# Optimization experiments

Measured on AMD Instinct MI355X. Metric: run time of the kernel, lower is better.

Reference implementation:

```python
import jax, jax.numpy as jnp
import numpy as np

NUM_HEADS = 16
HEAD_DIM = 64
BATCH = 4
SEQ = 1024
MAX_SEQ_LEN = 2048


def _shift(pos_score):
    # Transformer-XL relative shift. pos_score: (NH, S, S_kv)
    NH, S, S_kv = pos_score.shape
    zero_pad = jnp.zeros((NH, S, 1), dtype=pos_score.dtype)
    padded = jnp.concatenate([zero_pad, pos_score], axis=-1)  # (NH, S, S_kv+1)
    padded = padded.reshape(NH, S_kv + 1, S)
    return padded[:, 1:, :].reshape(NH, S, S_kv)


def setup_inputs() -> dict:
    key = jax.random.key(0)
    ks = jax.random.split(key, 6)
    NH = BATCH * NUM_HEADS
    return {
        "queries": jax.random.normal(ks[0], (NH, SEQ, HEAD_DIM), dtype=jnp.float32),
        "keys": jax.random.normal(ks[1], (NH, SEQ, HEAD_DIM), dtype=jnp.float32),
        "values": jax.random.normal(ks[2], (NH, SEQ, HEAD_DIM), dtype=jnp.float32),
        "u_bias": jax.random.normal(ks[3], (1, NUM_HEADS, 1, HEAD_DIM), dtype=jnp.float32),
        "v_bias": jax.random.normal(ks[4], (1, NUM_HEADS, 1, HEAD_DIM), dtype=jnp.float32),
        "R": jax.random.normal(ks[5], (NUM_HEADS, MAX_SEQ_LEN, HEAD_DIM), dtype=jnp.float32),
    }


def reference(queries, keys, values, u_bias, v_bias, R):
    NH, S, d = queries.shape
    S_kv = keys.shape[1]
    batch = NH // NUM_HEADS

    q = queries * (d ** -0.5)
    q = q.reshape(batch, NUM_HEADS, S, d)
    q_u = (q + u_bias).reshape(NH, S, d)
    q_v = (q + v_bias).reshape(NH, S, d)

    # relative position embeddings, tiled over batch: (NH, S_kv, d)
    R_s = jnp.tile(R[:, :S_kv, :], (batch, 1, 1))

    content_score = jnp.einsum('nsd,ntd->nst', q_u, keys)   # (NH, S, S_kv)
    pos_score = jnp.einsum('nsd,ntd->nst', q_v, R_s)        # (NH, S, S_kv)
    pos_score = _shift(pos_score)

    attn_weights = jax.nn.softmax(content_score + pos_score, axis=-1)
    attn = jnp.einsum('nst,ntd->nsd', attn_weights, values)  # (NH, S, d)
    return attn
```

## Files before the change

### kernel.cpp

```cpp
#include <hip/hip_runtime.h>


#define SQ    1024
#define HD    64
#define NHD   16
#define RMAX  2048

typedef _Float16 f16x8 __attribute__((ext_vector_type(8)));
typedef _Float16 f16x4 __attribute__((ext_vector_type(4)));
typedef short    b16x8 __attribute__((ext_vector_type(8)));
typedef short    b16x4 __attribute__((ext_vector_type(4)));
typedef float    f32x4 __attribute__((ext_vector_type(4)));
typedef unsigned u32x2 __attribute__((ext_vector_type(2)));

#define MFMA_F16(A,B,C)  __builtin_amdgcn_mfma_f32_16x16x32_f16((A),(B),(C),0,0,0)
#define MFMA_BF16(A,B,C) __builtin_amdgcn_mfma_f32_16x16x32_bf16((A),(B),(C),0,0,0)

#define L2E    1.44269504088896f
#define NSHIFT (-57.7078016f)

#define KH_OFF   0
#define VT_OFF   (8u << 20)
#define R16_OFF  (18u << 20)
#define WS_NEED  (20u << 20)

__device__ __forceinline__ float exp2fast(float x) {
#if __has_builtin(__builtin_amdgcn_exp2f)
  return __builtin_amdgcn_exp2f(x);
#else
  return __expf(x * 0.693147180559945f);
#endif
}

__device__ __forceinline__ f32x4 mfma16bf(b16x4 a, b16x4 b, f32x4 c) {
#if __has_builtin(__builtin_amdgcn_mfma_f32_16x16x16bf16_1k)
  return __builtin_amdgcn_mfma_f32_16x16x16bf16_1k(a, b, c, 0, 0, 0);
#else
  b16x8 az = {a[0], a[1], a[2], a[3], 0, 0, 0, 0};
  b16x8 bz = {b[0], b[1], b[2], b[3], 0, 0, 0, 0};
  return MFMA_BF16(az, bz, c);
#endif
}

__device__ __forceinline__ short f2b(float f) {
  unsigned u = __builtin_bit_cast(unsigned, f);
  u += 0x7FFFu + ((u >> 16) & 1u);
  return (short)(u >> 16);
}
__device__ __forceinline__ unsigned pkh(float a, float b) {
  _Float16 h0 = (_Float16)a, h1 = (_Float16)b;
  return (unsigned)__builtin_bit_cast(unsigned short, h0)
       | ((unsigned)__builtin_bit_cast(unsigned short, h1) << 16);
}
__device__ __forceinline__ unsigned pkb2(float a, float b) {
  unsigned ua = __builtin_bit_cast(unsigned, a) + 0x8000u;
  unsigned ub = __builtin_bit_cast(unsigned, b) + 0x8000u;
  return (ub & 0xFFFF0000u) | (ua >> 16);
}
__device__ __forceinline__ float h2f(unsigned w, int sh) {
  return (float)__builtin_bit_cast(_Float16, (unsigned short)(w >> sh));
}
__device__ __forceinline__ int swz(int row, int col) {
  return row*64 + ((((col >> 3) ^ row) & 7) << 3) + (col & 7);
}
__device__ __forceinline__ int swzv(int row, int col) {
  return row*64 + ((((col >> 3) ^ row) & 7) << 3)
       + ((col & 7) ^ ((row & 8) >> 1));
}


__global__ __launch_bounds__(256) void preprep(
    const float* __restrict__ K, const float* __restrict__ R,
    const float* __restrict__ V,
    _Float16* __restrict__ Kh, _Float16* __restrict__ R16,
    short* __restrict__ Vt)
{
  __shared__ float t[64][65];
  const int bid = blockIdx.x, tid = threadIdx.x;
  if (bid < 1024) {
    const int n = bid >> 4, st = bid & 15;
    {
      const int row = tid >> 2, c0 = (tid & 3) * 16;
      const float* src = V + ((size_t)n * SQ + st * 64 + row) * HD + c0;
#pragma unroll
      for (int i = 0; i < 4; ++i) {
        float4 x = ((const float4*)src)[i];
        t[row][c0 + 4*i + 0] = x.x; t[row][c0 + 4*i + 1] = x.y;
        t[row][c0 + 4*i + 2] = x.z; t[row][c0 + 4*i + 3] = x.w;
      }
    }
    __syncthreads();
    {
      const int d = tid >> 2, s0 = (tid & 3) * 16;
      short* dst = Vt + ((size_t)n * 80 + d) * SQ + st * 64 + s0;
#pragma unroll
      for (int i = 0; i < 8; ++i)
        *(unsigned*)(dst + 2*i) = pkb2(t[s0 + 2*i][d], t[s0 + 2*i + 1][d]);
    }
    if (tid < 64) {
      const int s = st * 64 + tid;
      Vt[((size_t)n * 80 + 64) * SQ + s] = (short)0x3F80;
#pragma unroll
      for (int r = 65; r < 80; ++r) Vt[((size_t)n * 80 + r) * SQ + s] = 0;
    }
  } else {
    const int idx = (bid - 1024) * 256 + tid;
    const int nk4 = (64 * SQ * HD) / 4;
    if (idx < nk4) {
      float4 v = ((const float4*)K)[idx];
      f16x4 o = { (_Float16)v.x, (_Float16)v.y, (_Float16)v.z, (_Float16)v.w };
      *(f16x4*)(Kh + 4 * (size_t)idx) = o;
    } else {
      int rr = idx - nk4;
      int h  = rr >> 14, off = rr & 16383;
      float4 v = ((const float4*)R)[((size_t)h << 15) + off];
      f16x4 o = { (_Float16)v.x, (_Float16)v.y, (_Float16)v.z, (_Float16)v.w };
      *(f16x4*)(R16 + 4 * (((size_t)h << 14) + off)) = o;
    }
  }
}


__global__ __launch_bounds__(256, 3) void relpos_sdpa_r16(
    const float* __restrict__ Q, const _Float16* __restrict__ Kh,
    const short* __restrict__ Vtg, const _Float16* __restrict__ R16,
    const float* __restrict__ Ub, const float* __restrict__ Vb,
    float* __restrict__ O)
{
  const int n    = blockIdx.x;
  const int h    = n & (NHD - 1);
  const int a0   = blockIdx.y * 64;
  const int tid  = threadIdx.x;
  const int lane = tid & 63, wave = tid >> 6;
  const int l15  = lane & 15, quad = lane >> 4;

  const float*    Qn  = Q   + (size_t)n * SQ * HD;
  const _Float16* Khn = Kh  + (size_t)n * SQ * HD;
  const short*    Vgn = Vtg + (size_t)n * 80 * SQ;
  const _Float16* Rh  = R16 + (size_t)h * SQ * HD;

  __shared__ __align__(16) char lds[33808];
  _Float16*       Kb   = (_Float16*)lds;
  short*          Vt   = (short*)(lds + 8192);
  unsigned*       Pb2  = (unsigned*)(lds + 16384);
  const _Float16* Pb2h = (const _Float16*)Pb2;

  f16x8 quF[2], qvF[5][2];
#pragma unroll
  for (int ks = 0; ks < 2; ++ks) {
    const int db = ks * 32 + quad * 8;
    float ub[8], vb[8];
#pragma unroll
    for (int j = 0; j < 8; ++j) {
      ub[j] = Ub[h*HD + db + j] * L2E;
      vb[j] = Vb[h*HD + db + j] * L2E;
    }
    {
      const float* p = Qn + (size_t)(a0 + 16*wave + l15) * HD + db;
      float4 x0 = ((const float4*)p)[0], x1 = ((const float4*)p)[1];
      f16x8 f;
#pragma unroll
      for (int t = 0; t < 4; ++t) {
        f[t]   = (_Float16)((&x0.x)[t] * (0.125f * L2E) + ub[t]);
        f[t+4] = (_Float16)((&x1.x)[t] * (0.125f * L2E) + ub[t+4]);
      }
      quF[ks] = f;
    }
#pragma unroll
    for (int rt = 0; rt < 5; ++rt) {
      int row = a0 + 16*rt + l15; if (row > SQ-1) row = SQ-1;
      const float* p = Qn + (size_t)row * HD + db;
      float4 x0 = ((const float4*)p)[0], x1 = ((const float4*)p)[1];
      f16x8 f;
#pragma unroll
      for (int t = 0; t < 4; ++t) {
        f[t]   = (_Float16)((&x0.x)[t] * (0.125f * L2E) + vb[t]);
        f[t+4] = (_Float16)((&x1.x)[t] * (0.125f * L2E) + vb[t+4]);
      }
      qvF[rt][ks] = f;
    }
  }

  f32x4 Oacc[4], acc_l;
#pragma unroll
  for (int ct = 0; ct < 4; ++ct) Oacc[ct] = (f32x4){0.f, 0.f, 0.f, 0.f};
  acc_l = (f32x4){0.f, 0.f, 0.f, 0.f};

  const b16x4 ONESB = {(short)0x3F80, (short)0x3F80, (short)0x3F80, (short)0x3F80};

  unsigned ringW[9];
  int ringSlot, ringSlotN;
  f16x8 bB0, bB1;
  auto bandLoad = [&](int jstart) {
    const int c = jstart + 16*wave + l15;
    const int j = (c + 2048) & (SQ - 1);
    ringSlotN   = (c + 2048) & 127;
    const _Float16* rp = Rh + (size_t)j * HD + quad * 8;
    bB0 = *(const f16x8*)rp;
    bB1 = *(const f16x8*)(rp + 32);
  };
  auto bandMFMA = [&]() {
    ringSlot = ringSlotN;
    __builtin_amdgcn_s_setprio(1);
#pragma unroll
    for (int rt = 0; rt < 5; ++rt) {
      f32x4 acc = (f32x4){0.f, 0.f, 0.f, 0.f};
      acc = MFMA_F16(qvF[rt][0], bB0, acc);
      acc = MFMA_F16(qvF[rt][1], bB1, acc);
      if (rt < 4) {
        ringW[2*rt]     = pkh(acc[0], acc[1]);
        ringW[2*rt + 1] = pkh(acc[2], acc[3]);
      } else {
        ringW[8] = pkh(acc[0], acc[1]);
      }
    }
    __builtin_amdgcn_s_setprio(0);
  };
  auto ringFlush = [&]() {
#pragma unroll
    for (int rt = 0; rt < 4; ++rt) {
      const int rp0 = 8*rt + 2*quad;
      Pb2[rp0*132 + ringSlot]       = ringW[2*rt];
      Pb2[(rp0 + 1)*132 + ringSlot] = ringW[2*rt + 1];
    }
    if (quad == 0) Pb2[32*132 + ringSlot] = ringW[8];
    if (ringSlot < 3) {
      const int ms = ringSlot + 128;
#pragma unroll
      for (int rt = 0; rt < 4; ++rt) {
        const int rp0 = 8*rt + 2*quad;
        Pb2[rp0*132 + ms]       = ringW[2*rt];
        Pb2[(rp0 + 1)*132 + ms] = ringW[2*rt + 1];
      }
      if (quad == 0) Pb2[32*132 + ms] = ringW[8];
    }
  };

  bandLoad(-a0 - 65);  bandMFMA();  ringFlush();
  bandLoad(-a0 - 1);   bandMFMA();  ringFlush();

  f16x8 kPre[2]; b16x8 vPre[2];
  auto stageLoad = [&](int k0) {
    const _Float16* ks = Khn + (size_t)(k0 + lane) * HD + wave*8;
    kPre[0] = *(const f16x8*)ks;
    kPre[1] = *(const f16x8*)(ks + 32);
    const short* vs = Vgn + (size_t)lane * SQ + k0 + wave*8;
    vPre[0] = *(const b16x8*)vs;
    vPre[1] = *(const b16x8*)(vs + 32);
  };
  auto stageWrite = [&]() {
    *(f16x8*)&Kb[swz(lane, wave*8)]      = kPre[0];
    *(f16x8*)&Kb[swz(lane, 32 + wave*8)] = kPre[1];
    const int hx = (lane & 8) >> 1;
    const int c0 = ((wave       ^ lane) & 7) << 3;
    const int c1 = (((wave + 4) ^ lane) & 7) << 3;
    short* vr = &Vt[lane * 64];
    b16x8 v0 = vPre[0], v1 = vPre[1];
    b16x4 v0lo = {v0[0], v0[1], v0[2], v0[3]};
    b16x4 v0hi = {v0[4], v0[5], v0[6], v0[7]};
    b16x4 v1lo = {v1[0], v1[1], v1[2], v1[3]};
    b16x4 v1hi = {v1[4], v1[5], v1[6], v1[7]};
    *(b16x4*)&vr[c0 + hx]       = v0lo;
    *(b16x4*)&vr[c0 + (4 ^ hx)] = v0hi;
    *(b16x4*)&vr[c1 + hx]       = v1lo;
    *(b16x4*)&vr[c1 + (4 ^ hx)] = v1hi;
  };

  stageLoad(0);

  const int iiB = 16*wave + 4*quad;
  const int iQ  = 16*wave + l15;

  for (int k0 = 0; k0 < SQ; k0 += 64) {
    __syncthreads();

    stageWrite();
    if (k0 > 0) ringFlush();

    __syncthreads();

    if (k0 < SQ - 64) {
      stageLoad(k0 + 64);
      bandLoad(k0 + 64 - a0 - 1);
    }

    f32x4 sc[4];
    __builtin_amdgcn_s_setprio(1);
#pragma unroll
    for (int ct = 0; ct < 4; ++ct) {
      f16x8 ka = *(const f16x8*)&Kb[swz(16*ct + l15, quad*8)];
      f16x8 kb = *(const f16x8*)&Kb[swz(16*ct + l15, 32 + quad*8)];
      f32x4 acc = (f32x4){NSHIFT, NSHIFT, NSHIFT, NSHIFT};
      acc = MFMA_F16(ka, quF[0], acc);
      acc = MFMA_F16(kb, quF[1], acc);
      sc[ct] = acc;
    }
    __builtin_amdgcn_s_setprio(0);

    const int base = k0 - a0 - 16*wave;
    if (k0 == a0 || k0 == a0 + 64) {
      const int adA = (iQ >> 1) * 264 + (iQ & 1);
      const int adB = ((iQ + 1) >> 1) * 264 + ((iQ + 1) & 1);
#pragma unroll
      for (int ct = 0; ct < 4; ++ct) {
        const int e0 = base + 16*ct + 4*quad - l15;
#pragma unroll
        for (int r = 0; r < 4; ++r) {
          const int e    = e0 + r;
          const int u    = (e > 0) ? 1 : 0;
          const int slot = (e - 1 - u) & 127;
          float pos = (float)Pb2h[(u ? adB : adA) + 2*slot];
          float s   = sc[ct][r] + ((e == 1) ? 0.f : pos);
          sc[ct][r] = exp2fast(s);
        }
      }
    } else {
      const int u  = (k0 > a0) ? 1 : 0;
      const int iu = iQ + u;
      const unsigned* wrow = &Pb2[(iu >> 1) * 132];
      const int sh = (iu & 1) << 4;
      const int sb = base - 1 - u + 4*quad - l15 + 2048;
#pragma unroll
      for (int ct = 0; ct < 4; ++ct) {
        const int s0 = (sb + 16*ct) & 127;
        unsigned w0 = wrow[s0];
        unsigned w1 = wrow[s0 + 1];
        unsigned w2 = wrow[s0 + 2];
        unsigned w3 = wrow[s0 + 3];
        sc[ct][0] = exp2fast(sc[ct][0] + h2f(w0, sh));
        sc[ct][1] = exp2fast(sc[ct][1] + h2f(w1, sh));
        sc[ct][2] = exp2fast(sc[ct][2] + h2f(w2, sh));
        sc[ct][3] = exp2fast(sc[ct][3] + h2f(w3, sh));
      }
    }

    __builtin_amdgcn_s_setprio(1);
#pragma unroll
    for (int ctk = 0; ctk < 4; ++ctk) {
      unsigned lo = pkb2(sc[ctk][0], sc[ctk][1]);
      unsigned hi = pkb2(sc[ctk][2], sc[ctk][3]);
      b16x4 aF = __builtin_bit_cast(b16x4, (u32x2){lo, hi});
      acc_l = mfma16bf(aF, ONESB, acc_l);
#pragma unroll
      for (int ctd = 0; ctd < 4; ++ctd) {
        b16x4 bF = *(const b16x4*)&Vt[swzv(16*ctd + l15, 16*ctk + 4*quad)];
        Oacc[ctd] = mfma16bf(aF, bF, Oacc[ctd]);
      }
    }
    __builtin_amdgcn_s_setprio(0);

    if (k0 < SQ - 64) bandMFMA();
  }

#pragma unroll
  for (int r = 0; r < 4; ++r) {
    float inv = 1.0f / acc_l[r];
    const size_t rowo = (size_t)n * SQ * HD + (size_t)(a0 + iiB + r) * HD;
#pragma unroll
    for (int ct = 0; ct < 4; ++ct)
      O[rowo + 16*ct + l15] = Oacc[ct][r] * inv;
  }
}


__global__ __launch_bounds__(256, 4) void relpos_sdpa_fb(
    const float* __restrict__ Q, const float* __restrict__ K,
    const float* __restrict__ V, const float* __restrict__ Ub,
    const float* __restrict__ Vb, const float* __restrict__ R,
    float* __restrict__ O)
{
  const int n    = blockIdx.x;
  const int h    = n & (NHD - 1);
  const int a0   = blockIdx.y * 64;
  const int tid  = threadIdx.x;
  const int lane = tid & 63, wave = tid >> 6;
  const int l15  = lane & 15, quad = lane >> 4;

  const float* Qn = Q + (size_t)n * SQ * HD;
  const float* Kn = K + (size_t)n * SQ * HD;
  const float* Vn = V + (size_t)n * SQ * HD;
  const float* Rh = R + (size_t)h * RMAX * HD;

  __shared__ __align__(16) char lds[38656];
  _Float16* Kb = (_Float16*)lds;
  short*    Ps = (short*)lds;
  short*    Vt = (short*)(lds + 9216);
  _Float16* Pb = (_Float16*)(lds + 9216 + 11520);

  f16x8 quF[2], qvF[5][2];
#pragma unroll
  for (int ks = 0; ks < 2; ++ks) {
    const int db = ks * 32 + quad * 8;
    float ub[8], vb[8];
#pragma unroll
    for (int j = 0; j < 8; ++j) { ub[j] = Ub[h*HD + db + j]; vb[j] = Vb[h*HD + db + j]; }
    {
      const float* p = Qn + (size_t)(a0 + 16*wave + l15) * HD + db;
      f16x8 f;
#pragma unroll
      for (int j = 0; j < 8; ++j) f[j] = (_Float16)(p[j] * 0.125f + ub[j]);
      quF[ks] = f;
    }
#pragma unroll
    for (int rt = 0; rt < 5; ++rt) {
      int row = a0 + 16*rt + l15; if (row > SQ-1) row = SQ-1;
      const float* p = Qn + (size_t)row * HD + db;
      f16x8 f;
#pragma unroll
      for (int j = 0; j < 8; ++j) f[j] = (_Float16)(p[j] * 0.125f + vb[j]);
      qvF[rt][ks] = f;
    }
  }

  if (tid < 64) Vt[64*72 + tid] = (short)0x3F80;

  f32x4 Oacc[5];
#pragma unroll
  for (int ct = 0; ct < 5; ++ct) Oacc[ct] = (f32x4){0.f, 0.f, 0.f, 0.f};

  auto band = [&](int jstart) {
    const int c    = jstart + 16*wave + l15;
    const int j    = (c + 2048) & (SQ - 1);
    const int slot = (c + 2048) & 127;
    const float* rp = Rh + (size_t)j * HD + quad * 8;
    f16x8 B0, B1;
    {
      float4 x0 = *(const float4*)(rp),      x1 = *(const float4*)(rp + 4);
      float4 y0 = *(const float4*)(rp + 32), y1 = *(const float4*)(rp + 36);
#pragma unroll
      for (int t = 0; t < 4; ++t) { B0[t] = (_Float16)(&x0.x)[t]; B0[t+4] = (_Float16)(&x1.x)[t]; }
#pragma unroll
      for (int t = 0; t < 4; ++t) { B1[t] = (_Float16)(&y0.x)[t]; B1[t+4] = (_Float16)(&y1.x)[t]; }
    }
#pragma unroll
    for (int rt = 0; rt < 5; ++rt) {
      f32x4 acc = (f32x4){0.f, 0.f, 0.f, 0.f};
      acc = MFMA_F16(qvF[rt][0], B0, acc);
      acc = MFMA_F16(qvF[rt][1], B1, acc);
      const int row = 16*rt + 4*quad;
      if (rt < 4) {
        *(unsigned*)&Pb[slot*70 + row]     = pkh(acc[0], acc[1]);
        *(unsigned*)&Pb[slot*70 + row + 2] = pkh(acc[2], acc[3]);
      } else if (quad == 0) {
        *(unsigned*)&Pb[slot*70 + row]     = pkh(acc[0], acc[1]);
      }
    }
  };

  band(-a0 - 65);
  band(-a0 - 1);

  const int sr = tid >> 2, sc4 = tid & 3;
  const int iiB = 16*wave + 4*quad;

  for (int k0 = 0; k0 < SQ; k0 += 64) {
    __syncthreads();
    {
      const float* src = Kn + (size_t)(k0 + sr) * HD + sc4 * 16;
      float4 x0 = *(const float4*)(src),     x1 = *(const float4*)(src + 4);
      float4 y0 = *(const float4*)(src + 8), y1 = *(const float4*)(src + 12);
      f16x8 lo, hi;
#pragma unroll
      for (int t = 0; t < 4; ++t) { lo[t] = (_Float16)(&x0.x)[t]; lo[t+4] = (_Float16)(&x1.x)[t]; }
#pragma unroll
      for (int t = 0; t < 4; ++t) { hi[t] = (_Float16)(&y0.x)[t]; hi[t+4] = (_Float16)(&y1.x)[t]; }
      *(f16x8*)&Kb[sr*72 + sc4*16]     = lo;
      *(f16x8*)&Kb[sr*72 + sc4*16 + 8] = hi;
    }
    {
      const int g = lane >> 3;
#pragma unroll
      for (int i = 0; i < 8; ++i) {
        int bp = 8*wave + (i ^ g);
        float v0 = Vn[(size_t)(k0 + 2*bp)     * HD + lane];
        float v1 = Vn[(size_t)(k0 + 2*bp + 1) * HD + lane];
        *(unsigned*)&Vt[lane*72 + 2*bp] = pkb2(v0, v1);
      }
    }
    __syncthreads();

    f32x4 sc[4];
#pragma unroll
    for (int ct = 0; ct < 4; ++ct) {
      f16x8 b0 = *(const f16x8*)&Kb[(16*ct + l15)*72 + quad*8];
      f16x8 b1 = *(const f16x8*)&Kb[(16*ct + l15)*72 + 32 + quad*8];
      f32x4 acc = (f32x4){0.f, 0.f, 0.f, 0.f};
      acc = MFMA_F16(quF[0], b0, acc);
      acc = MFMA_F16(quF[1], b1, acc);
      sc[ct] = acc;
    }

    const int dlt = k0 - a0;
#pragma unroll
    for (int r = 0; r < 4; ++r) {
      const int ii = iiB + r;
#pragma unroll
      for (int ct = 0; ct < 4; ++ct) {
        const int e    = dlt + 16*ct + l15 - ii;
        const int u    = (e > 0) ? 1 : 0;
        const int slot = (e - 1 - u + 2048) & 127;
        float pos = (float)Pb[slot*70 + ii + u];
        float s   = sc[ct][r] + ((e == 1) ? 0.f : pos);
        sc[ct][r] = __expf(s - 40.0f);
      }
    }
    __syncthreads();

#pragma unroll
    for (int r = 0; r < 4; ++r)
#pragma unroll
      for (int ct = 0; ct < 4; ++ct)
        Ps[(iiB + r)*68 + 16*ct + l15] = f2b(sc[ct][r]);

    b16x8 pA0 = *(const b16x8*)&Ps[(16*wave + l15)*68 + quad*8];
    b16x8 pA1 = *(const b16x8*)&Ps[(16*wave + l15)*68 + 32 + quad*8];
#pragma unroll
    for (int ct = 0; ct < 5; ++ct) {
      b16x8 v0 = *(const b16x8*)&Vt[(16*ct + l15)*72 + quad*8];
      b16x8 v1 = *(const b16x8*)&Vt[(16*ct + l15)*72 + 32 + quad*8];
      Oacc[ct] = MFMA_BF16(pA0, v0, Oacc[ct]);
      Oacc[ct] = MFMA_BF16(pA1, v1, Oacc[ct]);
    }

    if (k0 < SQ - 64) band(k0 + 64 - a0 - 1);
  }

#pragma unroll
  for (int r = 0; r < 4; ++r) {
    float l   = __shfl(Oacc[4][r], lane & 48);
    float inv = 1.0f / l;
    const size_t rowo = (size_t)n * SQ * HD + (size_t)(a0 + iiB + r) * HD;
#pragma unroll
    for (int ct = 0; ct < 4; ++ct)
      O[rowo + 16*ct + l15] = Oacc[ct][r] * inv;
  }
}

extern "C" void kernel_launch(void* const* d_in, const int* in_sizes, int n_in,
                              void* d_out, int out_size, void* d_ws, size_t ws_size,
                              hipStream_t stream) {
  const float* Q  = (const float*)d_in[0];
  const float* K  = (const float*)d_in[1];
  const float* V  = (const float*)d_in[2];
  const float* Ub = (const float*)d_in[3];
  const float* Vb = (const float*)d_in[4];
  const float* R  = (const float*)d_in[5];
  float* O = (float*)d_out;

  if (ws_size >= WS_NEED) {
    _Float16* Kh  = (_Float16*)((char*)d_ws + KH_OFF);
    short*    Vt  = (short*)((char*)d_ws + VT_OFF);
    _Float16* R16 = (_Float16*)((char*)d_ws + R16_OFF);

    preprep<<<6144, 256, 0, stream>>>(K, R, V, Kh, R16, Vt);

    dim3 grid(64, 16);
    relpos_sdpa_r16<<<grid, 256, 0, stream>>>(Q, Kh, Vt, R16, Ub, Vb, O);
  } else {
    dim3 grid(64, 16);
    relpos_sdpa_fb<<<grid, 256, 0, stream>>>(Q, K, V, Ub, Vb, R, O);
  }
}
```

Baseline: 169.9 us.

## Stream K/V tiles directly into double-buffered LDS with global_load_lds

Replaces the register-staged K/V tile loads and LDS writes with direct global-to-LDS DMA (global_load_lds) into two ping-pong buffers. Each loop iteration now issues the next tile's loads while computing on the current one, with explicit waitcnt/barrier placement. The V transpose kernel pre-applies the XOR swizzle so the DMA'd layout matches the LDS read pattern. LDS use grows from about 33.8 KB to 50 KB per block, which may reduce occupancy, and the hand-written vmcnt counts are fragile.

```diff
diff --git a/kernel.cpp b/kernel.cpp
--- a/kernel.cpp
+++ b/kernel.cpp
@@ -12,6 +12,7 @@
 typedef short    b16x4 __attribute__((ext_vector_type(4)));
 typedef float    f32x4 __attribute__((ext_vector_type(4)));
 typedef unsigned u32x2 __attribute__((ext_vector_type(2)));
+typedef unsigned u32x4 __attribute__((ext_vector_type(4)));
 
 #define MFMA_F16(A,B,C)  __builtin_amdgcn_mfma_f32_16x16x32_f16((A),(B),(C),0,0,0)
 #define MFMA_BF16(A,B,C) __builtin_amdgcn_mfma_f32_16x16x32_bf16((A),(B),(C),0,0,0)
@@ -92,10 +93,11 @@
     __syncthreads();
     {
       const int d = tid >> 2, s0 = (tid & 3) * 16;
+      const int xo = (d & 8) ? 4 : 0;
       short* dst = Vt + ((size_t)n * 80 + d) * SQ + st * 64 + s0;
 #pragma unroll
       for (int i = 0; i < 8; ++i)
-        *(unsigned*)(dst + 2*i) = pkb2(t[s0 + 2*i][d], t[s0 + 2*i + 1][d]);
+        *(unsigned*)(dst + (2*i ^ xo)) = pkb2(t[s0 + 2*i][d], t[s0 + 2*i + 1][d]);
     }
     if (tid < 64) {
       const int s = st * 64 + tid;
@@ -121,7 +123,7 @@
 }
 
 
-__global__ __launch_bounds__(256, 3) void relpos_sdpa_r16(
+__global__ __launch_bounds__(256, 3) void relpos_sdpa_r17(
     const float* __restrict__ Q, const _Float16* __restrict__ Kh,
     const short* __restrict__ Vtg, const _Float16* __restrict__ R16,
     const float* __restrict__ Ub, const float* __restrict__ Vb,
@@ -139,11 +141,34 @@
   const short*    Vgn = Vtg + (size_t)n * 80 * SQ;
   const _Float16* Rh  = R16 + (size_t)h * SQ * HD;
 
-  __shared__ __align__(16) char lds[33808];
-  _Float16*       Kb   = (_Float16*)lds;
-  short*          Vt   = (short*)(lds + 8192);
-  unsigned*       Pb2  = (unsigned*)(lds + 16384);
+  __shared__ __align__(16) char lds[50192];
+  unsigned*       Pb2  = (unsigned*)(lds + 32768);
   const _Float16* Pb2h = (const _Float16*)Pb2;
+
+  auto gload16 = [&](const void* g, void* l) {
+#if __has_builtin(__builtin_amdgcn_global_load_lds)
+    __builtin_amdgcn_global_load_lds(
+        (const __attribute__((address_space(1))) unsigned*)g,
+        (__attribute__((address_space(3))) unsigned*)l, 16, 0, 0);
+#else
+    *(u32x4*)((char*)l + lane * 16) = *(const u32x4*)g;
+#endif
+  };
+  auto dmaStage = [&](int kk, int buf) {
+    const int rb = lane >> 3;
+    const int g  = (lane & 7) ^ ((lane >> 3) & 7);
+    char* kdst = lds + buf * 8192;
+    char* vdst = lds + 16384 + buf * 8192;
+#pragma unroll
+    for (int i = 0; i < 2; ++i) {
+      const int sub = 2*wave + i;
+      const int r   = 8*sub + rb;
+      gload16(Khn + (size_t)(kk + r) * HD + 8*g, kdst + sub * 1024);
+      gload16(Vgn + (size_t)r * SQ + kk + 8*g,   vdst + sub * 1024);
+    }
+  };
+
+  dmaStage(0, 0);
 
   f16x8 quF[2], qvF[5][2];
 #pragma unroll
@@ -239,50 +264,31 @@
   bandLoad(-a0 - 65);  bandMFMA();  ringFlush();
   bandLoad(-a0 - 1);   bandMFMA();  ringFlush();
 
-  f16x8 kPre[2]; b16x8 vPre[2];
-  auto stageLoad = [&](int k0) {
-    const _Float16* ks = Khn + (size_t)(k0 + lane) * HD + wave*8;
-    kPre[0] = *(const f16x8*)ks;
-    kPre[1] = *(const f16x8*)(ks + 32);
-    const short* vs = Vgn + (size_t)lane * SQ + k0 + wave*8;
-    vPre[0] = *(const b16x8*)vs;
-    vPre[1] = *(const b16x8*)(vs + 32);
-  };
-  auto stageWrite = [&]() {
-    *(f16x8*)&Kb[swz(lane, wave*8)]      = kPre[0];
-    *(f16x8*)&Kb[swz(lane, 32 + wave*8)] = kPre[1];
-    const int hx = (lane & 8) >> 1;
-    const int c0 = ((wave       ^ lane) & 7) << 3;
-    const int c1 = (((wave + 4) ^ lane) & 7) << 3;
-    short* vr = &Vt[lane * 64];
-    b16x8 v0 = vPre[0], v1 = vPre[1];
-    b16x4 v0lo = {v0[0], v0[1], v0[2], v0[3]};
-    b16x4 v0hi = {v0[4], v0[5], v0[6], v0[7]};
-    b16x4 v1lo = {v1[0], v1[1], v1[2], v1[3]};
-    b16x4 v1hi = {v1[4], v1[5], v1[6], v1[7]};
-    *(b16x4*)&vr[c0 + hx]       = v0lo;
-    *(b16x4*)&vr[c0 + (4 ^ hx)] = v0hi;
-    *(b16x4*)&vr[c1 + hx]       = v1lo;
-    *(b16x4*)&vr[c1 + (4 ^ hx)] = v1hi;
-  };
-
-  stageLoad(0);
-
   const int iiB = 16*wave + 4*quad;
   const int iQ  = 16*wave + l15;
 
+  int cur = 0;
   for (int k0 = 0; k0 < SQ; k0 += 64) {
-    __syncthreads();
-
-    stageWrite();
+    __builtin_amdgcn_sched_barrier(0);
+    asm volatile("s_waitcnt lgkmcnt(0)" ::: "memory");
+    __builtin_amdgcn_s_barrier();
+    __builtin_amdgcn_sched_barrier(0);
+
     if (k0 > 0) ringFlush();
-
-    __syncthreads();
-
     if (k0 < SQ - 64) {
-      stageLoad(k0 + 64);
       bandLoad(k0 + 64 - a0 - 1);
-    }
+      dmaStage(k0 + 64, cur ^ 1);
+      __builtin_amdgcn_sched_barrier(0);
+      asm volatile("s_waitcnt vmcnt(6) lgkmcnt(0)" ::: "memory");
+    } else {
+      __builtin_amdgcn_sched_barrier(0);
+      asm volatile("s_waitcnt vmcnt(0) lgkmcnt(0)" ::: "memory");
+    }
+    __builtin_amdgcn_s_barrier();
+    __builtin_amdgcn_sched_barrier(0);
+
+    const _Float16* Kb = (const _Float16*)(lds + (cur << 13));
+    const short*    Vt = (const short*)(lds + 16384 + (cur << 13));
 
     f32x4 sc[4];
     __builtin_amdgcn_s_setprio(1);
@@ -350,6 +356,7 @@
     __builtin_amdgcn_s_setprio(0);
 
     if (k0 < SQ - 64) bandMFMA();
+    cur ^= 1;
   }
 
 #pragma unroll
@@ -555,7 +562,7 @@
     preprep<<<6144, 256, 0, stream>>>(K, R, V, Kh, R16, Vt);
 
     dim3 grid(64, 16);
-    relpos_sdpa_r16<<<grid, 256, 0, stream>>>(Q, Kh, Vt, R16, Ub, Vb, O);
+    relpos_sdpa_r17<<<grid, 256, 0, stream>>>(Q, Kh, Vt, R16, Ub, Vb, O);
   } else {
     dim3 grid(64, 16);
     relpos_sdpa_fb<<<grid, 256, 0, stream>>>(Q, K, V, Ub, Vb, R, O);
```

After: 167.9 us. No clear change (-1.2%).
